# Performance work log

Measured on AMD Instinct MI355X. Metric: run time of the kernel, lower is better.

## Reference

```python
import jax, jax.numpy as jnp
import numpy as np
from jax import lax

T_LOW, T_HIGH = 100.0, 200.0   # init kwargs of Canny
TG22 = 0.4142135623730951      # tan(22.5 deg), cv2's direction quantization constant
MAX_ITERS = 512                # safety cap on hysteresis fixed-point loop


def _shift(a, dy, dx):
    # neighbor value n[y, x] = a[y + dy, x + dx], zero outside
    H, W = a.shape
    p = jnp.pad(a, 1)
    return p[1 + dy:1 + dy + H, 1 + dx:1 + dx + W]


def _canny(x):
    B, C, H, W = x.shape
    # toRGB: ((x+1)/2*255).to(uint8)  (truncation; values are non-negative)
    img = jnp.clip(jnp.floor((x + 1.0) * 0.5 * 255.0), 0.0, 255.0)
    # original reshapes batch into one tall strip (B*H, W, C) before cv2.Canny
    img = img.transpose(0, 2, 3, 1).reshape(B * H, W, C)
    HH = B * H
    p = jnp.pad(img, ((1, 1), (1, 1), (0, 0)), mode='edge')  # replicate border like cv2

    def s(dy, dx):
        return p[1 + dy:1 + dy + HH, 1 + dx:1 + dx + W, :]

    # 3x3 Sobel per channel
    gx = (s(-1, 1) + 2.0 * s(0, 1) + s(1, 1)) - (s(-1, -1) + 2.0 * s(0, -1) + s(1, -1))
    gy = (s(1, -1) + 2.0 * s(1, 0) + s(1, 1)) - (s(-1, -1) + 2.0 * s(-1, 0) + s(-1, 1))
    mag_c = jnp.abs(gx) + jnp.abs(gy)  # L1 magnitude (cv2 default L2gradient=False)
    # multi-channel: take channel with max magnitude per pixel (cv2 behavior)
    idx = jnp.argmax(mag_c, axis=-1, keepdims=True)
    gx = jnp.take_along_axis(gx, idx, -1)[..., 0]
    gy = jnp.take_along_axis(gy, idx, -1)[..., 0]
    mag = jnp.take_along_axis(mag_c, idx, -1)[..., 0]

    # non-maximum suppression with 4 quantized directions
    ax_, ay_ = jnp.abs(gx), jnp.abs(gy)
    is_h = ay_ < TG22 * ax_          # gradient ~horizontal -> compare left/right
    is_v = ay_ * TG22 > ax_          # gradient ~vertical -> compare up/down
    same = (gx * gy) >= 0.0          # diagonal orientation by sign agreement
    n1 = jnp.where(is_h, _shift(mag, 0, -1),
         jnp.where(is_v, _shift(mag, -1, 0),
         jnp.where(same, _shift(mag, -1, -1), _shift(mag, -1, 1))))
    n2 = jnp.where(is_h, _shift(mag, 0, 1),
         jnp.where(is_v, _shift(mag, 1, 0),
         jnp.where(same, _shift(mag, 1, 1), _shift(mag, 1, -1))))
    keep = (mag > n1) & (mag >= n2)

    strong = keep & (mag > T_HIGH)
    weak = keep & (mag > T_LOW)

    # hysteresis: propagate strong labels through 8-connected weak pixels to fixed point
    def dilate(m):
        mf = m.astype(jnp.float32)
        return lax.reduce_window(mf, 0.0, lax.add, (3, 3), (1, 1), 'SAME') > 0.0

    def body(st):
        s0, _, it = st
        grown = (dilate(s0) & weak) | s0
        return grown, jnp.any(grown != s0), it + 1

    def cond(st):
        return st[1] & (st[2] < MAX_ITERS)

    strong, _, _ = lax.while_loop(cond, body, (strong, jnp.array(True), jnp.array(0)))

    edges = strong.reshape(B, H, W).astype(jnp.float32)        # {0,1} == cv2 {0,255}/255
    edges = jnp.broadcast_to(edges[:, None, :, :], (B, 3, H, W))
    return (edges - 0.5) / 0.5                                 # T.Normalize(0.5, 0.5)


def setup_inputs() -> dict:
    key = jax.random.key(0)
    x = jax.random.uniform(key, (16, 3, 512, 512), jnp.float32, -1.0, 1.0)
    return {"x": x}


def reference(x):
    return _canny(x)
```

## Files before the change

### kernel.cpp

```cpp
#include <hip/hip_runtime.h>
#include <stdint.h>

#define HH 8192
#define WW 512
#define WPR 8
#define TG22F 0.4142135623730951f
#define NSWEEP 8


__device__ __forceinline__ float to_img(float v) {
    float t = floorf((v + 1.0f) * 0.5f * 255.0f);
    return fminf(fmaxf(t, 0.0f), 255.0f);
}

__device__ __forceinline__ int bsel(uint64_t w0, uint64_t w1, int idx) {
    return (idx < 8) ? (int)((w0 >> (idx * 8)) & 255)
                     : (int)((w1 >> ((idx - 8) * 8)) & 255);
}

__device__ __forceinline__ uint64_t runfill(uint64_t s, uint64_t w) {
    uint64_t sw = s & w;
    uint64_t up = ((sw + w) ^ w) & w;
    uint64_t rs = __brevll(sw);
    uint64_t rw = __brevll(w);
    uint64_t dn = __brevll(((rs + rw) ^ rw) & rw);
    return up | dn | sw;
}

__global__ void k_sobel(const float* __restrict__ in, uint16_t* __restrict__ packed) {
    __shared__ uint8_t simg[3 * 34 * 72];
    const int tid = threadIdx.x;
    const int row0 = (blockIdx.x >> 3) << 5;
    const int col0 = (blockIdx.x & 7) << 6;

    for (int i = tid; i < 1632; i += 256) {
        int c = i / 544;
        int rem = i - c * 544;
        int hr = rem >> 4;
        int q = rem & 15;
        int gy = row0 + hr - 1;
        gy = gy < 0 ? 0 : (gy >= HH ? HH - 1 : gy);
        int b = gy >> 9, h = gy & 511;
        const float4 v = *(const float4*)&in[((((b * 3 + c) << 9) + h) << 9) + col0 + (q << 2)];
        uint32_t pk = (uint32_t)(uint8_t)to_img(v.x)
                    | ((uint32_t)(uint8_t)to_img(v.y) << 8)
                    | ((uint32_t)(uint8_t)to_img(v.z) << 16)
                    | ((uint32_t)(uint8_t)to_img(v.w) << 24);
        *(uint32_t*)&simg[(c * 34 + hr) * 72 + 4 + (q << 2)] = pk;
    }
    for (int i = tid; i < 204; i += 256) {
        int c = i / 68;
        int rem = i - c * 68;
        int hr = rem >> 1;
        int side = rem & 1;
        int gy = row0 + hr - 1;
        gy = gy < 0 ? 0 : (gy >= HH ? HH - 1 : gy);
        int gc = side ? col0 + 64 : col0 - 1;
        gc = gc < 0 ? 0 : (gc >= WW ? WW - 1 : gc);
        int b = gy >> 9, h = gy & 511;
        float v = to_img(in[((((b * 3 + c) << 9) + h) << 9) + gc]);
        simg[(c * 34 + hr) * 72 + (side ? 68 : 3)] = (uint8_t)v;
    }
    __syncthreads();

    const int r = tid >> 3;
    const int c8 = (tid & 7) << 3;

    int bestMag[8], bgx[8], bgy[8];
    #pragma unroll
    for (int j = 0; j < 8; ++j) { bestMag[j] = -1; bgx[j] = 0; bgy[j] = 0; }

    #pragma unroll
    for (int c = 0; c < 3; ++c) {
        const uint8_t* base = &simg[(c * 34 + r) * 72 + c8];
        uint64_t w00 = *(const uint64_t*)(base);
        uint64_t w01 = *(const uint64_t*)(base + 8);
        uint64_t w10 = *(const uint64_t*)(base + 72);
        uint64_t w11 = *(const uint64_t*)(base + 80);
        uint64_t w20 = *(const uint64_t*)(base + 144);
        uint64_t w21 = *(const uint64_t*)(base + 152);
        int vs[10], t0[10], t2[10];
        #pragma unroll
        for (int i = 0; i < 10; ++i) {
            int a0 = bsel(w00, w01, 3 + i);
            int a1 = bsel(w10, w11, 3 + i);
            int a2 = bsel(w20, w21, 3 + i);
            vs[i] = a0 + 2 * a1 + a2;
            t0[i] = a0; t2[i] = a2;
        }
        #pragma unroll
        for (int j = 0; j < 8; ++j) {
            int gx = vs[j + 2] - vs[j];
            int gy = (t2[j] + 2 * t2[j + 1] + t2[j + 2]) - (t0[j] + 2 * t0[j + 1] + t0[j + 2]);
            int mg = abs(gx) + abs(gy);
            if (mg > bestMag[j]) { bestMag[j] = mg; bgx[j] = gx; bgy[j] = gy; }
        }
    }

    uint32_t res[4];
    #pragma unroll
    for (int jj = 0; jj < 4; ++jj) {
        uint32_t pair = 0;
        #pragma unroll
        for (int s = 0; s < 2; ++s) {
            int j = jj * 2 + s;
            float axf = (float)abs(bgx[j]);
            float ayf = (float)abs(bgy[j]);
            int dir;
            if (ayf < TG22F * axf)      dir = 0;
            else if (ayf * TG22F > axf) dir = 1;
            else                        dir = (bgx[j] * bgy[j] >= 0) ? 2 : 3;
            uint32_t val = (uint32_t)(bestMag[j] | (dir << 12));
            pair |= val << (s * 16);
        }
        res[jj] = pair;
    }
    int y = row0 + r;
    *(uint4*)&packed[y * WW + col0 + c8] = *(uint4*)res;
}

__global__ void k_nms(const uint16_t* __restrict__ packed,
                      unsigned long long* __restrict__ strongB,
                      unsigned long long* __restrict__ weakB,
                      int* __restrict__ flags) {
    if (blockIdx.x == 0 && threadIdx.x < 16) flags[threadIdx.x] = 0;
    int y = blockIdx.x >> 1;
    int x = ((blockIdx.x & 1) << 8) + threadIdx.x;
    uint16_t own = packed[y * WW + x];
    int mag = own & 0xFFF;
    int dir = own >> 12;
    int d1y = (dir == 0) ? 0 : -1;
    int d1x = (dir == 0) ? -1 : (dir == 1) ? 0 : (dir == 2) ? -1 : 1;
    int n1y = y + d1y, n1x = x + d1x;
    int n2y = y - d1y, n2x = x - d1x;
    int n1 = (n1y >= 0 && n1y < HH && n1x >= 0 && n1x < WW) ? (packed[n1y * WW + n1x] & 0xFFF) : 0;
    int n2 = (n2y >= 0 && n2y < HH && n2x >= 0 && n2x < WW) ? (packed[n2y * WW + n2x] & 0xFFF) : 0;
    bool keep = (mag > n1) && (mag >= n2);
    bool strong = keep && (mag > 200);
    bool weak   = keep && (mag > 100);
    unsigned long long sb = __ballot(strong ? 1 : 0);
    unsigned long long wb = __ballot(weak ? 1 : 0);
    if ((threadIdx.x & 63) == 0) {
        int word = y * WPR + (x >> 6);
        strongB[word] = sb;
        weakB[word]   = wb;
    }
}

__global__ void __launch_bounds__(256) k_sweep(
        const unsigned long long* __restrict__ weakB,
        unsigned long long* __restrict__ buf,
        int* __restrict__ flags, int sidx)
{
    if (sidx > 0 && flags[sidx - 1] == 0) return;
    __shared__ uint64_t tA[66][8];
    __shared__ uint64_t tB[66][8];
    const int tid = threadIdx.x;
    const int b = blockIdx.x;
    const int r = tid >> 3;
    const int k = tid & 7;
    const int g0 = (b * 64 + r) * WPR + k;
    const int g1 = g0 + 32 * WPR;
    const uint64_t wk0 = weakB[g0];
    const uint64_t wk1 = weakB[g1];
    const uint64_t l0 = buf[g0];
    const uint64_t l1 = buf[g1];
    tA[r + 1][k]  = l0;
    tA[r + 33][k] = l1;
    if (tid < 8) {
        uint64_t h = (b > 0) ? buf[(b * 64 - 1) * WPR + tid] : 0ull;
        tA[0][tid] = h; tB[0][tid] = h;
    } else if (tid < 16) {
        int kk = tid - 8;
        uint64_t h = (b < 127) ? buf[(b * 64 + 64) * WPR + kk] : 0ull;
        tA[65][kk] = h; tB[65][kk] = h;
    }
    __syncthreads();

    uint64_t (*src)[8] = tA;
    uint64_t (*dst)[8] = tB;
    uint64_t o0 = l0, o1 = l1;
    for (;;) {
        uint64_t acc0 = 0, acc1 = 0;
        #pragma unroll
        for (int dr = 0; dr < 3; ++dr) {
            uint64_t c0v = src[r + dr][k];
            uint64_t h0 = c0v | (c0v << 1) | (c0v >> 1);
            if (k > 0) h0 |= src[r + dr][k - 1] >> 63;
            if (k < 7) h0 |= src[r + dr][k + 1] << 63;
            acc0 |= h0;
            uint64_t c1v = src[r + 32 + dr][k];
            uint64_t h1 = c1v | (c1v << 1) | (c1v >> 1);
            if (k > 0) h1 |= src[r + 32 + dr][k - 1] >> 63;
            if (k < 7) h1 |= src[r + 32 + dr][k + 1] << 63;
            acc1 |= h1;
        }
        uint64_t n0 = runfill(o0 | (acc0 & wk0), wk0);
        uint64_t n1 = runfill(o1 | (acc1 & wk1), wk1);
        dst[r + 1][k]  = n0;
        dst[r + 33][k] = n1;
        int any = __syncthreads_or((int)((n0 != o0) | (n1 != o1)));
        o0 = n0; o1 = n1;
        uint64_t (*t)[8] = src; src = dst; dst = t;
        if (!any) break;
    }
    bool ch = (o0 != l0) || (o1 != l1);
    if (o0 != l0) buf[g0] = o0;
    if (o1 != l1) buf[g1] = o1;
    if (__ballot(ch ? 1 : 0) != 0ull && (tid & 63) == 0)
        __hip_atomic_store(&flags[sidx], 1, __ATOMIC_RELAXED, __HIP_MEMORY_SCOPE_AGENT);
}

__global__ void k_out(const unsigned long long* __restrict__ result, float* __restrict__ out) {
    int t = blockIdx.x * blockDim.x + threadIdx.x;
    int b = t >> 16;
    int r = t & 65535;
    int h = r >> 7;
    int w = (r & 127) << 2;
    int y = (b << 9) + h;
    unsigned long long word = result[y * WPR + (w >> 6)];
    int sh = w & 63;
    float4 v;
    v.x = ((word >> (sh + 0)) & 1ull) ? 1.0f : -1.0f;
    v.y = ((word >> (sh + 1)) & 1ull) ? 1.0f : -1.0f;
    v.z = ((word >> (sh + 2)) & 1ull) ? 1.0f : -1.0f;
    v.w = ((word >> (sh + 3)) & 1ull) ? 1.0f : -1.0f;
    int base = (b * 3) << 18;
    int off = (h << 9) + w;
    *(float4*)&out[base + off] = v;
    *(float4*)&out[base + 262144 + off] = v;
    *(float4*)&out[base + 524288 + off] = v;
}

extern "C" void kernel_launch(void* const* d_in, const int* in_sizes, int n_in,
                              void* d_out, int out_size, void* d_ws, size_t ws_size,
                              hipStream_t stream) {
    const float* x = (const float*)d_in[0];
    float* out = (float*)d_out;
    char* ws = (char*)d_ws;

    uint16_t* packed          = (uint16_t*)(ws);
    unsigned long long* buf   = (unsigned long long*)(ws + 8388608);
    unsigned long long* weakB = (unsigned long long*)(ws + 8912896);
    int* flags                = (int*)(ws + 9437184);

    k_sobel<<<2048, 256, 0, stream>>>(x, packed);
    k_nms<<<HH * 2, 256, 0, stream>>>(packed, buf, weakB, flags);
    for (int s = 0; s < NSWEEP; ++s)
        k_sweep<<<128, 256, 0, stream>>>(weakB, buf, flags, s);
    k_out<<<4096, 256, 0, stream>>>(buf, out);
}
```

Measured before the change: 139.9 us.

## Fuse NMS into the first hysteresis sweep and cut the sweep launch count

The per-pixel NMS kernel is merged into the first hysteresis sweep. Each of 128 blocks loads a 68-row packed magnitude/direction tile into shared memory, computes strong/weak bitmasks with ballots for its 64 rows plus a one-row halo, and runs the local propagation loop without a global round-trip. The flag reset moves into the Sobel kernel, and the follow-up sweep launches drop from 8 to 5. This removes one kernel launch and the global write and read of the bitmasks. The cost is much lower parallelism in the NMS phase (128 blocks instead of 16384) and a large shared-memory footprint per block.

```diff
diff --git a/kernel.cpp b/kernel.cpp
--- a/kernel.cpp
+++ b/kernel.cpp
@@ -5,7 +5,7 @@
 #define WW 512
 #define WPR 8
 #define TG22F 0.4142135623730951f
-#define NSWEEP 8
+#define NPOST 5
 
 
 __device__ __forceinline__ float to_img(float v) {
@@ -27,11 +27,14 @@
     return up | dn | sw;
 }
 
-__global__ void k_sobel(const float* __restrict__ in, uint16_t* __restrict__ packed) {
+__global__ void k_sobel(const float* __restrict__ in, uint16_t* __restrict__ packed,
+                        int* __restrict__ flags) {
     __shared__ uint8_t simg[3 * 34 * 72];
     const int tid = threadIdx.x;
     const int row0 = (blockIdx.x >> 3) << 5;
     const int col0 = (blockIdx.x & 7) << 6;
+
+    if (blockIdx.x == 0 && tid < 16) flags[tid] = 0;
 
     for (int i = tid; i < 1632; i += 256) {
         int c = i / 544;
@@ -119,32 +122,106 @@
     *(uint4*)&packed[y * WW + col0 + c8] = *(uint4*)res;
 }
 
-__global__ void k_nms(const uint16_t* __restrict__ packed,
-                      unsigned long long* __restrict__ strongB,
-                      unsigned long long* __restrict__ weakB,
-                      int* __restrict__ flags) {
-    if (blockIdx.x == 0 && threadIdx.x < 16) flags[threadIdx.x] = 0;
-    int y = blockIdx.x >> 1;
-    int x = ((blockIdx.x & 1) << 8) + threadIdx.x;
-    uint16_t own = packed[y * WW + x];
-    int mag = own & 0xFFF;
-    int dir = own >> 12;
-    int d1y = (dir == 0) ? 0 : -1;
-    int d1x = (dir == 0) ? -1 : (dir == 1) ? 0 : (dir == 2) ? -1 : 1;
-    int n1y = y + d1y, n1x = x + d1x;
-    int n2y = y - d1y, n2x = x - d1x;
-    int n1 = (n1y >= 0 && n1y < HH && n1x >= 0 && n1x < WW) ? (packed[n1y * WW + n1x] & 0xFFF) : 0;
-    int n2 = (n2y >= 0 && n2y < HH && n2x >= 0 && n2x < WW) ? (packed[n2y * WW + n2x] & 0xFFF) : 0;
-    bool keep = (mag > n1) && (mag >= n2);
-    bool strong = keep && (mag > 200);
-    bool weak   = keep && (mag > 100);
-    unsigned long long sb = __ballot(strong ? 1 : 0);
-    unsigned long long wb = __ballot(weak ? 1 : 0);
-    if ((threadIdx.x & 63) == 0) {
-        int word = y * WPR + (x >> 6);
-        strongB[word] = sb;
-        weakB[word]   = wb;
-    }
+__global__ void __launch_bounds__(256) k_nms_sweep(
+        const uint16_t* __restrict__ packed,
+        unsigned long long* __restrict__ buf,
+        unsigned long long* __restrict__ weakB,
+        int* __restrict__ flags)
+{
+    __shared__ uint16_t spad[68][512];
+    __shared__ uint64_t tA[66][8];
+    __shared__ uint64_t tB[66][8];
+    __shared__ uint64_t wwd[64][8];
+
+    const int tid = threadIdx.x;
+    const int b = blockIdx.x;
+    const int lane = tid & 63;
+    const int wave = tid >> 6;
+
+    for (int i = tid; i < 4352; i += 256) {
+        int row = i >> 6;
+        int x0 = (i & 63) << 3;
+        int y = b * 64 - 2 + row;
+        uint4 v = {0u, 0u, 0u, 0u};
+        if (y >= 0 && y < HH) v = *(const uint4*)&packed[y * WW + x0];
+        *(uint4*)&spad[row][x0] = v;
+    }
+    __syncthreads();
+
+    for (int t = wave; t < 528; t += 4) {
+        int row_m = t >> 3;
+        int k = t & 7;
+        int y = b * 64 - 1 + row_m;
+        int ry = row_m + 1;
+        int x = (k << 6) + lane;
+        uint16_t own = spad[ry][x];
+        int mag = own & 0xFFF;
+        int dir = own >> 12;
+        int d1y = (dir == 0) ? 0 : -1;
+        int d1x = (dir == 0) ? -1 : (dir == 1) ? 0 : (dir == 2) ? -1 : 1;
+        int n1y = y + d1y, n1x = x + d1x;
+        int n2y = y - d1y, n2x = x - d1x;
+        int n1 = (n1y >= 0 && n1y < HH && n1x >= 0 && n1x < WW)
+                 ? (spad[ry + d1y][n1x] & 0xFFF) : 0;
+        int n2 = (n2y >= 0 && n2y < HH && n2x >= 0 && n2x < WW)
+                 ? (spad[ry - d1y][n2x] & 0xFFF) : 0;
+        bool keep = (mag > n1) && (mag >= n2);
+        bool strong = keep && (mag > 200);
+        bool weak   = keep && (mag > 100);
+        unsigned long long sb = __ballot(strong ? 1 : 0);
+        unsigned long long wb = __ballot(weak ? 1 : 0);
+        if (lane == 0) {
+            tA[row_m][k] = sb;
+            if (row_m >= 1 && row_m <= 64) wwd[row_m - 1][k] = wb;
+        }
+    }
+    __syncthreads();
+
+    const int r = tid >> 3;
+    const int k = tid & 7;
+    const int g0 = (b * 64 + r) * WPR + k;
+    const int g1 = g0 + 32 * WPR;
+    const uint64_t wk0 = wwd[r][k];
+    const uint64_t wk1 = wwd[r + 32][k];
+    const uint64_t l0 = tA[r + 1][k];
+    const uint64_t l1 = tA[r + 33][k];
+    if (tid < 8)       tB[0][tid] = tA[0][tid];
+    else if (tid < 16) tB[65][tid - 8] = tA[65][tid - 8];
+
+    uint64_t (*src)[8] = tA;
+    uint64_t (*dst)[8] = tB;
+    uint64_t o0 = l0, o1 = l1;
+    for (;;) {
+        uint64_t acc0 = 0, acc1 = 0;
+        #pragma unroll
+        for (int dr = 0; dr < 3; ++dr) {
+            uint64_t c0v = src[r + dr][k];
+            uint64_t h0 = c0v | (c0v << 1) | (c0v >> 1);
+            if (k > 0) h0 |= src[r + dr][k - 1] >> 63;
+            if (k < 7) h0 |= src[r + dr][k + 1] << 63;
+            acc0 |= h0;
+            uint64_t c1v = src[r + 32 + dr][k];
+            uint64_t h1 = c1v | (c1v << 1) | (c1v >> 1);
+            if (k > 0) h1 |= src[r + 32 + dr][k - 1] >> 63;
+            if (k < 7) h1 |= src[r + 32 + dr][k + 1] << 63;
+            acc1 |= h1;
+        }
+        uint64_t n0 = runfill(o0 | (acc0 & wk0), wk0);
+        uint64_t n1 = runfill(o1 | (acc1 & wk1), wk1);
+        dst[r + 1][k]  = n0;
+        dst[r + 33][k] = n1;
+        int any = __syncthreads_or((int)((n0 != o0) | (n1 != o1)));
+        o0 = n0; o1 = n1;
+        uint64_t (*t)[8] = src; src = dst; dst = t;
+        if (!any) break;
+    }
+    buf[g0] = o0;
+    buf[g1] = o1;
+    weakB[g0] = wk0;
+    weakB[g1] = wk1;
+    bool ch = (o0 != l0) || (o1 != l1);
+    if (__ballot(ch ? 1 : 0) != 0ull && (tid & 63) == 0)
+        __hip_atomic_store(&flags[0], 1, __ATOMIC_RELAXED, __HIP_MEMORY_SCOPE_AGENT);
 }
 
 __global__ void __launch_bounds__(256) k_sweep(
@@ -152,7 +229,7 @@
         unsigned long long* __restrict__ buf,
         int* __restrict__ flags, int sidx)
 {
-    if (sidx > 0 && flags[sidx - 1] == 0) return;
+    if (flags[sidx - 1] == 0) return;
     __shared__ uint64_t tA[66][8];
     __shared__ uint64_t tB[66][8];
     const int tid = threadIdx.x;
@@ -244,9 +321,9 @@
     unsigned long long* weakB = (unsigned long long*)(ws + 8912896);
     int* flags                = (int*)(ws + 9437184);
 
-    k_sobel<<<2048, 256, 0, stream>>>(x, packed);
-    k_nms<<<HH * 2, 256, 0, stream>>>(packed, buf, weakB, flags);
-    for (int s = 0; s < NSWEEP; ++s)
+    k_sobel<<<2048, 256, 0, stream>>>(x, packed, flags);
+    k_nms_sweep<<<128, 256, 0, stream>>>(packed, buf, weakB, flags);
+    for (int s = 1; s <= NPOST; ++s)
         k_sweep<<<128, 256, 0, stream>>>(weakB, buf, flags, s);
     k_out<<<4096, 256, 0, stream>>>(buf, out);
 }
```

Measured after the change: 166.4 us. 1.19x slower.
